# Kernel optimization log

Hardware: AMD Instinct MI355X
Metric: run time of the kernel (lower is better)

The kernel has to match this reference:

```python
import jax, jax.numpy as jnp
import numpy as np

SCALE = 2      # shuffle_scale
K = 3          # nearest neighbors / conv kernel size (stride == K)
SAMPLES = 16   # sample grid size per axis -> M = SAMPLES**2


def pixel_unshuffle(x, s):
    B, C, H, W = x.shape
    x = x.reshape(B, C, H // s, s, W // s, s)
    x = x.transpose(0, 1, 3, 5, 2, 4)
    return x.reshape(B, C * s * s, H // s, W // s)


def pixel_shuffle(x, s):
    B, C, H, W = x.shape
    x = x.reshape(B, C // (s * s), s, s, H, W)
    x = x.transpose(0, 1, 4, 2, 5, 3)
    return x.reshape(B, C // (s * s), H * s, W * s)


def setup_inputs() -> dict:
    key = jax.random.key(0)
    k1, k2, k3 = jax.random.split(key, 3)
    x = jax.random.normal(k1, (32, 16, 128, 128), dtype=jnp.float32)
    weight = jax.random.normal(k2, (64, 64, K), dtype=jnp.float32) * 0.05  # [out_1d, in_1d, K]
    bias = jax.random.normal(k3, (64,), dtype=jnp.float32) * 0.05
    return {"x": x, "weight": weight, "bias": bias}


def reference(x, weight, bias):
    # --- pixel unshuffle ('B' part of 'BA') ---
    x1 = pixel_unshuffle(x, SCALE)                 # [B, C1=64, H1=64, W1=64]
    B, C1, H1, W1 = x1.shape
    N = H1 * W1

    # --- spatial subsample grid (linspace + round, sample_padding=0) ---
    xi = jnp.round(jnp.linspace(0.0, H1 - 1.0, SAMPLES)).astype(jnp.int32)
    yi = jnp.round(jnp.linspace(0.0, W1 - 1.0, SAMPLES)).astype(jnp.int32)
    xg, yg = jnp.meshgrid(xi, yi, indexing="ij")
    x_sample = x1[:, :, xg, yg].reshape(B, C1, -1)  # [B, C1, M]
    x2 = x1.reshape(B, C1, N)                       # [B, C1, N]

    # --- pairwise squared euclidean distance tokens -> samples ---
    # (sqrt omitted: monotone; top-k uses only indices, matching torch topk(largest=False))
    n2 = jnp.sum(x2 * x2, axis=1)                   # [B, N]
    m2 = jnp.sum(x_sample * x_sample, axis=1)       # [B, M]
    dot = jnp.einsum("bcn,bcm->bnm", x2, x_sample)  # [B, N, M]
    d2 = n2[:, :, None] + m2[:, None, :] - 2.0 * dot

    # --- K nearest sampled points per token ---
    _, idx = jax.lax.top_k(-d2, K)                  # [B, N, K]

    # --- gather neighbor features ('prime'); equals x2 at flat_indices[idx] ---
    prime = jnp.take_along_axis(x_sample[:, :, None, :], idx[:, None, :, :], axis=3)  # [B, C1, N, K]

    # --- Conv1d(kernel=K, stride=K) over [B, C1, N*K] == per-token contraction ---
    out = jnp.einsum("bcnk,ock->bon", prime, weight) + bias[None, :, None]  # [B, O1=64, N]
    out = out.reshape(B, weight.shape[0], H1, W1)

    # --- pixel shuffle ('A' part of 'BA') ---
    return pixel_shuffle(out, SCALE)                # [B, 16, 128, 128]
```

## Files before the change

kernel.cpp:

```cpp
#include <hip/hip_runtime.h>
#include <cstdint>
#include <cfloat>

typedef float v2f __attribute__((ext_vector_type(2)));

__constant__ int c_smp[16] = {0,4,8,13,17,21,25,29,34,38,42,46,50,55,59,63};

static constexpr int NB   = 32;
static constexpr int NC   = 64;
static constexpr int NH   = 64;
static constexpr int NTOK = 4096;
static constexpr int NM   = 256;
static constexpr int NK   = 3;

__global__ __launch_bounds__(256) void k_pre(const float* __restrict__ x,
                                             const float* __restrict__ w,
                                             float* __restrict__ wT,
                                             float* __restrict__ xs_t,
                                             float* __restrict__ xs_m) {
    __shared__ __align__(16) float rows[16][2][128];
    if (blockIdx.x >= NB * 16) {
        int f = (blockIdx.x - NB * 16) * 256 + threadIdx.x;
        float v = w[f];
        int o = f / 192, rem = f % 192;
        int c = rem / 3, k = rem % 3;
        wT[((size_t)k * 64 + c) * 64 + o] = v;
        return;
    }
    int b = blockIdx.x >> 4, gi = blockIdx.x & 15;
    int hh = c_smp[gi];
    int t = threadIdx.x;
    const float* xb = x + (size_t)b * 16 * 128 * 128;
#pragma unroll
    for (int it = 0; it < 4; ++it) {
        int q = t + it * 256;
        int c = q >> 6;
        int rem = q & 63;
        int sh = rem >> 5;
        int col = (rem & 31) * 4;
        float4 v = *(const float4*)(xb + ((size_t)c * 128 + (2 * hh + sh)) * 128 + col);
        *(float4*)&rows[c][sh][col] = v;
    }
    __syncthreads();
    {
        int c1 = t >> 2;
        int c = c1 >> 2, sh = (c1 >> 1) & 1, sw = c1 & 1;
        int gj0 = (t & 3) * 4;
        float4 v;
        v.x = rows[c][sh][2 * c_smp[gj0 + 0] + sw];
        v.y = rows[c][sh][2 * c_smp[gj0 + 1] + sw];
        v.z = rows[c][sh][2 * c_smp[gj0 + 2] + sw];
        v.w = rows[c][sh][2 * c_smp[gj0 + 3] + sw];
        *(float4*)&xs_t[((size_t)b * NC + c1) * NM + gi * 16 + gj0] = v;
    }
    {
        int mloc = t >> 4, cg = t & 15;
        int w2 = 2 * c_smp[mloc];
        float4 v;
        v.x = rows[cg][0][w2];
        v.y = rows[cg][0][w2 + 1];
        v.z = rows[cg][1][w2];
        v.w = rows[cg][1][w2 + 1];
        *(float4*)&xs_m[((size_t)b * NM + gi * 16 + mloc) * NC + cg * 4] = v;
    }
}

static __device__ __forceinline__ unsigned long long packkey(float d, int m) {
    unsigned u = __float_as_uint(d);
    u ^= ((unsigned)((int)u >> 31)) | 0x80000000u;
    return ((unsigned long long)u << 32) | (unsigned)m;
}

__global__ __launch_bounds__(256) void k_mid(const float* __restrict__ x,
                                             const float* __restrict__ xs_t,
                                             const float* __restrict__ xs_m,
                                             const float* __restrict__ wT,
                                             float* __restrict__ Z,
                                             int* __restrict__ idx) {
    __shared__ __align__(16) float att[16][64];
    __shared__ __align__(16) float xsB[16][256];
    __shared__ __align__(16) float m2l[256];
    __shared__ __align__(16) float n2l[64];

    if (blockIdx.x >= NB * 64) {
        int job = (blockIdx.x - NB * 64) * 4 + (threadIdx.x >> 6);
        int mg  = job & 15;
        int k   = (job >> 4) % 3;
        int b   = job / 48;
        int o   = threadIdx.x & 63;
        float wf[64];
#pragma unroll
        for (int c = 0; c < 64; ++c) wf[c] = wT[((size_t)k * 64 + c) * 64 + o];
        const float* xb = xs_m + (size_t)b * NM * NC;
        float* zb = Z + ((size_t)b * 3 + k) * NM * NC;
        for (int mm = 0; mm < 16; ++mm) {
            int m = mg * 16 + mm;
            const float* xr = xb + (size_t)m * NC;
            float acc = 0.f;
#pragma unroll
            for (int c = 0; c < 64; ++c) acc = fmaf(wf[c], xr[c], acc);
            zb[(size_t)m * NC + o] = acc;
        }
        return;
    }

    int b = blockIdx.x >> 6;
    int h = blockIdx.x & 63;
    int t = threadIdx.x;
    int r = t >> 4, cl = t & 15;

    v2f acc2[4][8];
#pragma unroll
    for (int i = 0; i < 4; ++i)
#pragma unroll
        for (int j = 0; j < 8; ++j) acc2[i][j] = (v2f)(0.f);

    float m2acc = 0.f, n2acc = 0.f;
    const float* xb = x + (size_t)b * 16 * 128 * 128;
    const float* xsb = xs_t + (size_t)b * NC * NM;

    for (int kc = 0; kc < 4; ++kc) {
        __syncthreads();
#pragma unroll
        for (int it = 0; it < 2; ++it) {
            int i = t + it * 256;
            int p = i >> 6;
            int wcol = i & 63;
            int c1e = kc * 16 + p * 2;
            int c = c1e >> 2, sh = (c1e >> 1) & 1;
            const float* src = xb + ((size_t)c * 128 + (2 * h + sh)) * 128 + 2 * wcol;
            float2 v = *(const float2*)src;
            att[p * 2 + 0][wcol] = v.x;
            att[p * 2 + 1][wcol] = v.y;
        }
#pragma unroll
        for (int it = 0; it < 4; ++it) {
            int g = t + it * 256;
            int row = g >> 6;
            int m4 = g & 63;
            int dst = ((((m4 & 3) << 4) | (m4 >> 2))) << 2;
            *(float4*)&xsB[row][dst] =
                *(const float4*)&xsb[(size_t)(kc * 16 + row) * NM + m4 * 4];
        }
        __syncthreads();

#pragma unroll
        for (int c = 0; c < 16; ++c) {
            float v = xsB[c][t];
            m2acc = __fadd_rn(m2acc, __fmul_rn(v, v));
        }
        if (t < 64) {
#pragma unroll
            for (int c = 0; c < 16; ++c) {
                float v = att[c][t];
                n2acc = __fadd_rn(n2acc, __fmul_rn(v, v));
            }
        }

#pragma unroll
        for (int k = 0; k < 16; ++k) {
            float4 a0 = *(const float4*)&att[k][r * 4];
            float4 b0 = *(const float4*)&xsB[k][(0 * 16 + cl) * 4];
            float4 b1 = *(const float4*)&xsB[k][(1 * 16 + cl) * 4];
            float4 b2 = *(const float4*)&xsB[k][(2 * 16 + cl) * 4];
            float4 b3 = *(const float4*)&xsB[k][(3 * 16 + cl) * 4];
            v2f bp0 = {b0.x, b0.y}, bp1 = {b0.z, b0.w};
            v2f bp2 = {b1.x, b1.y}, bp3 = {b1.z, b1.w};
            v2f bp4 = {b2.x, b2.y}, bp5 = {b2.z, b2.w};
            v2f bp6 = {b3.x, b3.y}, bp7 = {b3.z, b3.w};
            float aa[4] = {a0.x, a0.y, a0.z, a0.w};
#pragma unroll
            for (int i = 0; i < 4; ++i) {
                v2f ai = {aa[i], aa[i]};
                acc2[i][0] = __builtin_elementwise_fma(ai, bp0, acc2[i][0]);
                acc2[i][1] = __builtin_elementwise_fma(ai, bp1, acc2[i][1]);
                acc2[i][2] = __builtin_elementwise_fma(ai, bp2, acc2[i][2]);
                acc2[i][3] = __builtin_elementwise_fma(ai, bp3, acc2[i][3]);
                acc2[i][4] = __builtin_elementwise_fma(ai, bp4, acc2[i][4]);
                acc2[i][5] = __builtin_elementwise_fma(ai, bp5, acc2[i][5]);
                acc2[i][6] = __builtin_elementwise_fma(ai, bp6, acc2[i][6]);
                acc2[i][7] = __builtin_elementwise_fma(ai, bp7, acc2[i][7]);
            }
        }
    }

    m2l[((t >> 2) & 15) * 16 + (t >> 6) * 4 + (t & 3)] = m2acc;
    if (t < 64) n2l[t] = n2acc;
    __syncthreads();

    float m2r[16];
#pragma unroll
    for (int j = 0; j < 16; ++j) m2r[j] = m2l[cl * 16 + j];

#pragma unroll
    for (int i = 0; i < 4; ++i) {
        int nloc = r * 4 + i;
        float n2v = n2l[nloc];
        float e0d = FLT_MAX, e1d = FLT_MAX, e2d = FLT_MAX;
        int e0m = 0x7fffffff, e1m = 0x7fffffff, e2m = 0x7fffffff;
#pragma unroll
        for (int j = 0; j < 16; ++j) {
            float dv = acc2[i][j >> 1][j & 1];
            float t1 = __fadd_rn(n2v, m2r[j]);
            float d = __fadd_rn(t1, -2.0f * dv);
            int m = cl * 16 + j;
            if (d < e2d) {
                e2d = d; e2m = m;
                if (e2d < e1d) {
                    float td = e1d; int tm = e1m; e1d = e2d; e1m = e2m;
                    e2d = td; e2m = tm;
                    if (e1d < e0d) {
                        float sd = e0d; int sm = e0m; e0d = e1d; e0m = e1m;
                        e1d = sd; e1m = sm;
                    }
                }
            }
        }
        unsigned long long k0 = packkey(e0d, e0m);
        unsigned long long k1 = packkey(e1d, e1m);
        unsigned long long k2 = packkey(e2d, e2m);
#pragma unroll
        for (int mask = 1; mask <= 8; mask <<= 1) {
            unsigned long long q0 = __shfl_xor(k0, mask);
            unsigned long long q1 = __shfl_xor(k1, mask);
            unsigned long long q2 = __shfl_xor(k2, mask);
            unsigned long long clo = k0 < q0 ? k0 : q0;
            unsigned long long chi = k0 < q0 ? q0 : k0;
            unsigned long long dlo = k1 < q1 ? k1 : q1;
            unsigned long long dhi = k1 < q1 ? q1 : k1;
            unsigned long long f2  = k2 < q2 ? k2 : q2;
            unsigned long long elo = chi < dlo ? chi : dlo;
            unsigned long long ehi = chi < dlo ? dlo : chi;
            unsigned long long g2  = dhi < f2 ? dhi : f2;
            k0 = clo;
            k1 = elo;
            k2 = ehi < g2 ? ehi : g2;
        }
        if (cl == 0) {
            int n = h * 64 + nloc;
            int* op = idx + ((size_t)b * NTOK + n) * NK;
            op[0] = (int)(unsigned)(k0 & 0xffffffffu);
            op[1] = (int)(unsigned)(k1 & 0xffffffffu);
            op[2] = (int)(unsigned)(k2 & 0xffffffffu);
        }
    }
}

__global__ __launch_bounds__(256) void k_out(const float* __restrict__ Z,
                                             const int* __restrict__ idx,
                                             const float* __restrict__ bias,
                                             float* __restrict__ out) {
    __shared__ float staged[64 * 65];
    int b = blockIdx.x >> 6, h = blockIdx.x & 63;
    int t = threadIdx.x;
    int o = t & 63, wv = t >> 6;
    float bv = bias[o];
    const float* zb = Z + (size_t)b * 3 * NM * NC;
    const int* ib = idx + (size_t)b * NTOK * NK;
    for (int ti = 0; ti < 16; ++ti) {
        int w = wv * 16 + ti;
        int n = h * 64 + w;
        const int* ip = ib + (size_t)n * NK;
        int i0 = ip[0], i1 = ip[1], i2 = ip[2];
        float v = bv + zb[(size_t)i0 * NC + o]
                     + zb[(size_t)(NM + i1) * NC + o]
                     + zb[(size_t)(2 * NM + i2) * NC + o];
        staged[o * 65 + w] = v;
    }
    __syncthreads();
    float* ob = out + (size_t)b * 16 * 128 * 128;
#pragma unroll
    for (int it = 0; it < 16; ++it) {
        int flat = t + it * 256;
        int W = flat & 127, sh = (flat >> 7) & 1, cc = flat >> 8;
        int oo = cc * 4 + sh * 2 + (W & 1);
        ob[((size_t)cc * 128 + 2 * h + sh) * 128 + W] = staged[oo * 65 + (W >> 1)];
    }
}

extern "C" void kernel_launch(void* const* d_in, const int* in_sizes, int n_in,
                              void* d_out, int out_size, void* d_ws, size_t ws_size,
                              hipStream_t stream) {
    const float* x    = (const float*)d_in[0];
    const float* w    = (const float*)d_in[1];
    const float* bias = (const float*)d_in[2];
    float* out = (float*)d_out;
    float* ws  = (float*)d_ws;

    float* xs_t = ws;
    float* xs_m = ws + 524288;
    float* Z    = ws + 1048576;
    int*   idxb = (int*)(ws + 2621440);
    float* wT   = ws + 3014656;

    hipLaunchKernelGGL(k_pre, dim3(NB * 16 + 48),        dim3(256), 0, stream,
                       x, w, wT, xs_t, xs_m);
    hipLaunchKernelGGL(k_mid, dim3(NB * 64 + NB * 3 * 4), dim3(256), 0, stream,
                       x, xs_t, xs_m, wT, Z, idxb);
    hipLaunchKernelGGL(k_out, dim3(NB * 64),             dim3(256), 0, stream,
                       Z, idxb, bias, out);
}
```

Baseline: 189.1 us.

## Split sample-projection GEMM into tiled LDS kernel separate from distance kernel

The per-sample weight projection Z used to be computed by extra blocks inside the distance kernel, one thread per output with 64 weights held in registers and scalar loads of xs_m. It now runs in its own kernel that stages the weights and xs_t tiles in shared memory and computes a 4x4 register tile per thread with packed FMAs. This drops the xs_m layout and its writes in k_pre. The aim is to remove the register-heavy tail blocks that unbalanced the fused kernel. The cost is one extra kernel launch and serialisation, since Z is no longer computed in parallel with the distance work.

```diff
diff --git a/kernel.cpp b/kernel.cpp
--- a/kernel.cpp
+++ b/kernel.cpp
@@ -16,8 +16,7 @@
 __global__ __launch_bounds__(256) void k_pre(const float* __restrict__ x,
                                              const float* __restrict__ w,
                                              float* __restrict__ wT,
-                                             float* __restrict__ xs_t,
-                                             float* __restrict__ xs_m) {
+                                             float* __restrict__ xs_t) {
     __shared__ __align__(16) float rows[16][2][128];
     if (blockIdx.x >= NB * 16) {
         int f = (blockIdx.x - NB * 16) * 256 + threadIdx.x;
@@ -53,15 +52,61 @@
         v.w = rows[c][sh][2 * c_smp[gj0 + 3] + sw];
         *(float4*)&xs_t[((size_t)b * NC + c1) * NM + gi * 16 + gj0] = v;
     }
-    {
-        int mloc = t >> 4, cg = t & 15;
-        int w2 = 2 * c_smp[mloc];
-        float4 v;
-        v.x = rows[cg][0][w2];
-        v.y = rows[cg][0][w2 + 1];
-        v.z = rows[cg][1][w2];
-        v.w = rows[cg][1][w2 + 1];
-        *(float4*)&xs_m[((size_t)b * NM + gi * 16 + mloc) * NC + cg * 4] = v;
+}
+
+__global__ __launch_bounds__(256) void k_z2(const float* __restrict__ xs_t,
+                                            const float* __restrict__ wT,
+                                            float* __restrict__ Z) {
+    __shared__ __align__(16) float wL[64][64];
+    __shared__ __align__(16) float xt[16][64];
+    int bid = blockIdx.x;
+    int mq = bid & 3;
+    int k  = (bid >> 2) % 3;
+    int b  = bid / 12;
+    int t  = threadIdx.x;
+    int mg = t >> 4, og = t & 15;
+
+#pragma unroll
+    for (int it = 0; it < 4; ++it) {
+        int q = t + it * 256;
+        int c = q >> 4;
+        int o4 = (q & 15) * 4;
+        *(float4*)&wL[c][o4] = *(const float4*)&wT[(size_t)k * 4096 + q * 4];
+    }
+
+    v2f acc[4][2];
+#pragma unroll
+    for (int i = 0; i < 4; ++i) { acc[i][0] = (v2f)(0.f); acc[i][1] = (v2f)(0.f); }
+
+    for (int cc = 0; cc < 4; ++cc) {
+        __syncthreads();
+        {
+            int c = t >> 4, m4 = (t & 15) * 4;
+            *(float4*)&xt[c][m4] =
+                *(const float4*)&xs_t[((size_t)b * NC + cc * 16 + c) * NM + mq * 64 + m4];
+        }
+        __syncthreads();
+#pragma unroll
+        for (int c = 0; c < 16; ++c) {
+            float4 a4 = *(const float4*)&xt[c][mg * 4];
+            float4 b4 = *(const float4*)&wL[cc * 16 + c][og * 4];
+            v2f bp0 = {b4.x, b4.y}, bp1 = {b4.z, b4.w};
+            float aa[4] = {a4.x, a4.y, a4.z, a4.w};
+#pragma unroll
+            for (int i = 0; i < 4; ++i) {
+                v2f ai = {aa[i], aa[i]};
+                acc[i][0] = __builtin_elementwise_fma(ai, bp0, acc[i][0]);
+                acc[i][1] = __builtin_elementwise_fma(ai, bp1, acc[i][1]);
+            }
+        }
+    }
+
+    float* zb = Z + (((size_t)b * 3 + k) * NM + mq * 64) * NC;
+#pragma unroll
+    for (int i = 0; i < 4; ++i) {
+        int m = mg * 4 + i;
+        float4 v = {acc[i][0][0], acc[i][0][1], acc[i][1][0], acc[i][1][1]};
+        *(float4*)&zb[(size_t)m * NC + og * 4] = v;
     }
 }
 
@@ -71,38 +116,13 @@
     return ((unsigned long long)u << 32) | (unsigned)m;
 }
 
-__global__ __launch_bounds__(256) void k_mid(const float* __restrict__ x,
-                                             const float* __restrict__ xs_t,
-                                             const float* __restrict__ xs_m,
-                                             const float* __restrict__ wT,
-                                             float* __restrict__ Z,
-                                             int* __restrict__ idx) {
+__global__ __launch_bounds__(256) void k_dist(const float* __restrict__ x,
+                                              const float* __restrict__ xs_t,
+                                              int* __restrict__ idx) {
     __shared__ __align__(16) float att[16][64];
     __shared__ __align__(16) float xsB[16][256];
     __shared__ __align__(16) float m2l[256];
     __shared__ __align__(16) float n2l[64];
-
-    if (blockIdx.x >= NB * 64) {
-        int job = (blockIdx.x - NB * 64) * 4 + (threadIdx.x >> 6);
-        int mg  = job & 15;
-        int k   = (job >> 4) % 3;
-        int b   = job / 48;
-        int o   = threadIdx.x & 63;
-        float wf[64];
-#pragma unroll
-        for (int c = 0; c < 64; ++c) wf[c] = wT[((size_t)k * 64 + c) * 64 + o];
-        const float* xb = xs_m + (size_t)b * NM * NC;
-        float* zb = Z + ((size_t)b * 3 + k) * NM * NC;
-        for (int mm = 0; mm < 16; ++mm) {
-            int m = mg * 16 + mm;
-            const float* xr = xb + (size_t)m * NC;
-            float acc = 0.f;
-#pragma unroll
-            for (int c = 0; c < 64; ++c) acc = fmaf(wf[c], xr[c], acc);
-            zb[(size_t)m * NC + o] = acc;
-        }
-        return;
-    }
 
     int b = blockIdx.x >> 6;
     int h = blockIdx.x & 63;
@@ -288,15 +308,16 @@
     float* ws  = (float*)d_ws;
 
     float* xs_t = ws;
-    float* xs_m = ws + 524288;
-    float* Z    = ws + 1048576;
-    int*   idxb = (int*)(ws + 2621440);
-    float* wT   = ws + 3014656;
-
-    hipLaunchKernelGGL(k_pre, dim3(NB * 16 + 48),        dim3(256), 0, stream,
-                       x, w, wT, xs_t, xs_m);
-    hipLaunchKernelGGL(k_mid, dim3(NB * 64 + NB * 3 * 4), dim3(256), 0, stream,
-                       x, xs_t, xs_m, wT, Z, idxb);
-    hipLaunchKernelGGL(k_out, dim3(NB * 64),             dim3(256), 0, stream,
+    float* Z    = ws + 524288;
+    int*   idxb = (int*)(ws + 2097152);
+    float* wT   = ws + 2490368;
+
+    hipLaunchKernelGGL(k_pre,  dim3(NB * 16 + 48), dim3(256), 0, stream,
+                       x, w, wT, xs_t);
+    hipLaunchKernelGGL(k_z2,   dim3(NB * 3 * 4),   dim3(256), 0, stream,
+                       xs_t, wT, Z);
+    hipLaunchKernelGGL(k_dist, dim3(NB * 64),      dim3(256), 0, stream,
+                       x, xs_t, idxb);
+    hipLaunchKernelGGL(k_out,  dim3(NB * 64),      dim3(256), 0, stream,
                        Z, idxb, bias, out);
 }
```

Measured after the change: 172.7 us. -8.6%, faster.
